# Performance work log

Measured on AMD Instinct MI355X. Metric: run time of the kernel, lower is better.

## Reference

```python
import jax, jax.numpy as jnp
import numpy as np

N_DRUG, N_MICROBE = 1500, 1572
N = N_DRUG + N_MICROBE          # 3072 nodes
F_IN = 1546                     # raw feature dim (fc1: 1546 -> 256)
D0 = 256                        # GCN input dim after fc1
H1 = H2 = 128                   # GCN hidden dims (H1 + H2 = 256)
B = 16384                       # number of (left,right) query pairs


def _sym_norm(A):
    # D^{-1/2} A D^{-1/2} (no self loops), zeros kept for isolated nodes
    deg = A.sum(axis=1)
    d = jnp.where(deg > 0, jax.lax.rsqrt(deg), 0.0)
    return A * d[:, None] * d[None, :]


def _compute_inf(adj, L):
    # dl.compute_inf: L-hop influence = L-th power of sym-normalized adjacency
    An = _sym_norm(adj)
    M = An
    for _ in range(L - 1):
        M = M @ An
    return M


def _gcn_norm(W):
    # GCNConv normalization: add self loops (weight 1), sym-normalize by weighted degree
    Ahat = W + jnp.eye(W.shape[0], dtype=W.dtype)
    deg = Ahat.sum(axis=1)
    d = jnp.where(deg > 0, jax.lax.rsqrt(deg), 0.0)
    return Ahat * d[:, None] * d[None, :]


def _glorot(key, shape):
    return jax.random.normal(key, shape, dtype=jnp.float32) / np.sqrt(shape[0])


def setup_inputs() -> dict:
    key = jax.random.key(0)
    ks = jax.random.split(key, 24)
    u = jax.random.uniform(ks[0], (N, N), dtype=jnp.float32)
    w = jax.random.uniform(ks[1], (N, N), dtype=jnp.float32)
    adj = jnp.where(u < 0.01, w, 0.0)
    adj = jnp.maximum(adj, adj.T)
    X = jax.random.normal(ks[2], (N, F_IN), dtype=jnp.float32)
    left = jax.random.randint(ks[3], (B,), 0, N)
    right = jax.random.randint(ks[4], (B,), 0, N)
    return dict(
        left=left, right=right, X=X, adj=adj, threshold=jnp.float32(1e-4),
        W_fc1=_glorot(ks[5], (F_IN, D0)), b_fc1=jnp.zeros((D0,), jnp.float32),
        Wg1=_glorot(ks[6], (D0, H1)), bg1=jnp.zeros((H1,), jnp.float32),
        Wg2=_glorot(ks[7], (H1, H2)), bg2=jnp.zeros((H2,), jnp.float32),
        Wg3=_glorot(ks[8], (D0, H1)), bg3=jnp.zeros((H1,), jnp.float32),
        Wg4=_glorot(ks[9], (H1, H2)), bg4=jnp.zeros((H2,), jnp.float32),
        Wg5=_glorot(ks[10], (D0, H1)), bg5=jnp.zeros((H1,), jnp.float32),
        Wg6=_glorot(ks[11], (H1, H2)), bg6=jnp.zeros((H2,), jnp.float32),
        cnn_k=jax.random.normal(ks[12], (1, 3, 3, 3), dtype=jnp.float32) * 0.1,
        cnn_b=jnp.zeros((1,), jnp.float32),
        W_a=_glorot(ks[13], (2 * (H1 + H2), 64)), b_a=jnp.zeros((64,), jnp.float32),
        W_b=_glorot(ks[14], (64, 2)), b_b=jnp.zeros((2,), jnp.float32),
    )


def reference(left, right, X, adj, threshold,
              W_fc1, b_fc1, Wg1, bg1, Wg2, bg2, Wg3, bg3, Wg4, bg4,
              Wg5, bg5, Wg6, bg6, cnn_k, cnn_b, W_a, b_a, W_b, b_b):
    X0 = jax.nn.relu(X @ W_fc1 + b_fc1)  # fc1: [N, 1546] -> [N, 256]

    def branch(mask_src, Wa, ba, Wb, bb):
        # dynamically thresholded edges carry the ORIGINAL adj weights
        Wadj = jnp.where(mask_src > threshold, adj, 0.0)
        An = _gcn_norm(Wadj)                       # [N, N]
        e1 = jax.nn.relu(An @ (X0 @ Wa) + ba)      # GCNConv 1
        e2 = jax.nn.relu(An @ (e1 @ Wb) + bb)      # GCNConv 2
        return jnp.concatenate([e1, e2], axis=1)   # [N, 256]

    emb_l2 = branch(_compute_inf(adj, 2), Wg1, bg1, Wg2, bg2)
    emb_l1 = branch(_compute_inf(adj, 1), Wg3, bg3, Wg4, bg4)
    emb_l0 = branch(adj, Wg5, bg5, Wg6, bg6)

    emb = jnp.stack([emb_l0, emb_l1, emb_l2], axis=0)[None]  # [1, 3, N, 256]
    conv = jax.lax.conv_general_dilated(
        emb, cnn_k, window_strides=(1, 1), padding=[(2, 2), (2, 2)],
        rhs_dilation=(2, 2), dimension_numbers=('NCHW', 'OIHW', 'NCHW'))
    emb_all = conv[0, 0] + cnn_b[0]                # [N, 256]

    pair = jnp.concatenate([emb_all[left], emb_all[right]], axis=1)  # [B, 512]
    h = jax.nn.relu(pair @ W_a + b_a)              # dropout is identity at eval
    logits = h @ W_b + b_b                         # [B, 2]
    return logits, emb_all
```

## Files before the change

kernel.cpp:

```cpp
#include <hip/hip_runtime.h>

#define NN 3072
#define FIN 1546
#define KP 1568
#define MAXR 192
#define KSPLIT 7
#define KSLICE 224

#define WSPLIT_BLOCKS (256 * KP / 256)
#define WGA_BLOCKS 384
#define CSR_BLOCKS (NN / 4)
#define FC1_BLOCKS (48 * 4 * KSPLIT)
#define RED_BLOCKS 768

typedef __attribute__((ext_vector_type(8))) __bf16 bf16x8;
typedef __attribute__((ext_vector_type(4))) __bf16 bf16x4;
typedef __attribute__((ext_vector_type(4))) float f32x4;

__global__ __launch_bounds__(256) void prep_k(const float* __restrict__ adj,
                                              int* __restrict__ cols, float* __restrict__ vals,
                                              int* __restrict__ cnt, float* __restrict__ dvec,
                                              const float* __restrict__ W,
                                              __bf16* __restrict__ WhT, __bf16* __restrict__ WlT,
                                              const float* __restrict__ Wga0,
                                              const float* __restrict__ Wga1,
                                              const float* __restrict__ Wga2,
                                              __bf16* __restrict__ WgaTh, __bf16* __restrict__ WgaTl) {
    int bid = blockIdx.x;
    if (bid < WSPLIT_BLOCKS) {
        int idx = bid * 256 + threadIdx.x;
        int c = idx / KP, k = idx - c * KP;
        float x = (k < FIN) ? W[(size_t)k * 256 + c] : 0.f;
        __bf16 h = (__bf16)x;
        WhT[idx] = h;
        WlT[idx] = (__bf16)(x - (float)h);
        return;
    }
    bid -= WSPLIT_BLOCKS;
    if (bid < WGA_BLOCKS) {
        int idx = bid * 256 + threadIdx.x;
        int b = idx >> 15, r = idx & 32767;
        int c = r >> 8, k = r & 255;
        const float* Wp = (b == 0) ? Wga0 : (b == 1) ? Wga1 : Wga2;
        float x = Wp[k * 128 + c];
        __bf16 h = (__bf16)x;
        WgaTh[idx] = h;
        WgaTl[idx] = (__bf16)(x - (float)h);
        return;
    }
    bid -= WGA_BLOCKS;
    int i = bid * 4 + (threadIdx.x >> 6);
    int lane = threadIdx.x & 63;
    const float* row = adj + (size_t)i * NN;
    unsigned long long below = (1ull << lane) - 1ull;
    float s = 0.f; int count = 0;
    int base = i * MAXR;
    float4 a4 = *(const float4*)(row + lane * 4);
    for (int c0 = 0; c0 < NN; c0 += 256) {
        float4 nxt;
        if (c0 + 256 < NN) nxt = *(const float4*)(row + c0 + 256 + lane * 4);
        float a[4] = {a4.x, a4.y, a4.z, a4.w};
        s += a[0] + a[1] + a[2] + a[3];
        unsigned long long bal[4];
        #pragma unroll
        for (int u = 0; u < 4; u++) bal[u] = __ballot(a[u] != 0.f);
        int before = 0;
        #pragma unroll
        for (int u = 0; u < 4; u++) before += __popcll(bal[u] & below);
        int local = 0;
        #pragma unroll
        for (int u = 0; u < 4; u++) {
            if (a[u] != 0.f) {
                int pos = count + before + local;
                if (pos < MAXR) { cols[base + pos] = c0 + lane * 4 + u; vals[base + pos] = a[u]; }
                local++;
            }
        }
        int tot = 0;
        #pragma unroll
        for (int u = 0; u < 4; u++) tot += __popcll(bal[u]);
        count += tot;
        a4 = nxt;
    }
    for (int off = 32; off; off >>= 1) s += __shfl_xor(s, off);
    if (lane == 0) {
        cnt[i] = count < MAXR ? count : MAXR;
        dvec[i] = (s > 0.f) ? 1.0f / sqrtf(s) : 0.f;
    }
}

__global__ __launch_bounds__(256) void fc1mask01_k(const float* __restrict__ X,
                                                   const __bf16* __restrict__ WhT,
                                                   const __bf16* __restrict__ WlT,
                                                   float* __restrict__ Cpart,
                                                   const int* __restrict__ cols,
                                                   const float* __restrict__ vals,
                                                   const int* __restrict__ cnt,
                                                   const float* __restrict__ dvec,
                                                   const float* __restrict__ thrp,
                                                   int* __restrict__ mcols,
                                                   float* __restrict__ mvals,
                                                   int* __restrict__ mcnt,
                                                   float* __restrict__ db) {
    __shared__ float ds[256];
    __shared__ int lcnt;
    int bid = blockIdx.x, tid = threadIdx.x;

    if (bid < FC1_BLOCKS) {
        int bx = bid % 48;
        int byz = bid / 48;
        int by = byz % 4, z = byz / 4;
        int w = tid >> 6, lane = tid & 63;
        int m = lane & 15, q = lane >> 4;
        int i0 = bx * 64, c0 = by * 64;
        int k0 = z * KSLICE;
        int rowA = i0 + w * 16 + m;
        const float* xrow = X + (size_t)rowA * FIN + k0 + q * 8;
        const __bf16* bh0 = WhT + (size_t)(c0 + m) * KP + k0 + q * 8;
        const __bf16* bl0 = WlT + (size_t)(c0 + m) * KP + k0 + q * 8;

        f32x4 acc[4];
        #pragma unroll
        for (int ct = 0; ct < 4; ct++)
            #pragma unroll
            for (int r = 0; r < 4; r++) acc[ct][r] = 0.f;

        #pragma unroll 2
        for (int ks = 0; ks < KSLICE; ks += 32) {
            float xv[8];
            if (z < KSPLIT - 1) {
                const float2* xp = (const float2*)(xrow + ks);
                float2 p0 = xp[0], p1 = xp[1], p2 = xp[2], p3 = xp[3];
                xv[0] = p0.x; xv[1] = p0.y; xv[2] = p1.x; xv[3] = p1.y;
                xv[4] = p2.x; xv[5] = p2.y; xv[6] = p3.x; xv[7] = p3.y;
            } else {
                int kb = k0 + q * 8 + ks;
                #pragma unroll
                for (int e = 0; e < 8; e++)
                    xv[e] = (kb + e < FIN) ? xrow[ks + e] : 0.f;
            }
            bf16x8 ah, al;
            #pragma unroll
            for (int e = 0; e < 8; e++) {
                __bf16 h = (__bf16)xv[e];
                ah[e] = h;
                al[e] = (__bf16)(xv[e] - (float)h);
            }
            #pragma unroll
            for (int ct = 0; ct < 4; ct++) {
                bf16x8 bh = *(const bf16x8*)(bh0 + (size_t)ct * 16 * KP + ks);
                bf16x8 bl = *(const bf16x8*)(bl0 + (size_t)ct * 16 * KP + ks);
                acc[ct] = __builtin_amdgcn_mfma_f32_16x16x32_bf16(ah, bh, acc[ct], 0, 0, 0);
                acc[ct] = __builtin_amdgcn_mfma_f32_16x16x32_bf16(ah, bl, acc[ct], 0, 0, 0);
                acc[ct] = __builtin_amdgcn_mfma_f32_16x16x32_bf16(al, bh, acc[ct], 0, 0, 0);
            }
        }
        float* outp = Cpart + (size_t)z * NN * 256;
        int rowBase = i0 + w * 16 + q * 4;
        #pragma unroll
        for (int ct = 0; ct < 4; ct++) {
            int col = c0 + ct * 16 + m;
            #pragma unroll
            for (int r = 0; r < 4; r++)
                outp[(size_t)(rowBase + r) * 256 + col] = acc[ct][r];
        }
        return;
    }

    int t = bid - FC1_BLOCKS;
    int mode = (t < NN) ? 0 : 1;
    int i = (t < NN) ? t : t - NN;

    mcols += (size_t)mode * NN * MAXR;
    mvals += (size_t)mode * NN * MAXR;
    mcnt  += (size_t)mode * NN;
    db    += (size_t)mode * NN;
    int ni = cnt[i], base = i * MAXR;
    float thr = *thrp;
    float di = dvec[i];

    if (tid == 0) lcnt = 0;
    __syncthreads();
    float s = 0.f;
    if (tid < ni) {
        int j = cols[base + tid];
        float a = vals[base + tid];
        float mv = (mode == 0) ? a : a * di * dvec[j];
        if (mv > thr) {
            int p = atomicAdd(&lcnt, 1);
            mcols[base + p] = j;
            mvals[base + p] = a;
            s = a;
        }
    }
    ds[tid] = s; __syncthreads();
    for (int off = 128; off; off >>= 1) {
        if (tid < off) ds[tid] += ds[tid + off];
        __syncthreads();
    }
    if (tid == 0) {
        mcnt[i] = lcnt;
        db[i] = 1.0f / sqrtf(ds[0] + 1.0f);
    }
}

__global__ __launch_bounds__(256) void redm2_k(const float* __restrict__ Cpart,
                                               const float* __restrict__ bias,
                                               __bf16* __restrict__ X0h,
                                               __bf16* __restrict__ X0l,
                                               const int* __restrict__ cols,
                                               const float* __restrict__ vals,
                                               const int* __restrict__ cnt,
                                               const float* __restrict__ dvec,
                                               const float* __restrict__ thrp,
                                               int* __restrict__ mcols,
                                               float* __restrict__ mvals,
                                               int* __restrict__ mcnt,
                                               float* __restrict__ db) {
    __shared__ float ds[NN];
    __shared__ int lcols[MAXR];
    __shared__ float lvals[MAXR];
    __shared__ int lcnt;
    __shared__ float osum;
    int bid = blockIdx.x, tid = threadIdx.x;

    if (bid < RED_BLOCKS) {
        int idx4 = bid * 256 + tid;
        int i = idx4 >> 6, c4 = (idx4 & 63) << 2;
        float4 s = ((const float4*)Cpart)[idx4];
        #pragma unroll
        for (int z = 1; z < KSPLIT; z++) {
            float4 t4 = ((const float4*)(Cpart + (size_t)z * NN * 256))[idx4];
            s.x += t4.x; s.y += t4.y; s.z += t4.z; s.w += t4.w;
        }
        float4 b = *(const float4*)&bias[c4];
        s.x = fmaxf(s.x + b.x, 0.f); s.y = fmaxf(s.y + b.y, 0.f);
        s.z = fmaxf(s.z + b.z, 0.f); s.w = fmaxf(s.w + b.w, 0.f);
        __bf16 h0 = (__bf16)s.x, h1 = (__bf16)s.y, h2 = (__bf16)s.z, h3 = (__bf16)s.w;
        bf16x4 hv = {h0, h1, h2, h3};
        bf16x4 lv = {(__bf16)(s.x - (float)h0), (__bf16)(s.y - (float)h1),
                     (__bf16)(s.z - (float)h2), (__bf16)(s.w - (float)h3)};
        *(bf16x4*)(X0h + (size_t)i * 256 + c4) = hv;
        *(bf16x4*)(X0l + (size_t)i * 256 + c4) = lv;
        return;
    }

    int i = bid - RED_BLOCKS;
    mcols += (size_t)2 * NN * MAXR;
    mvals += (size_t)2 * NN * MAXR;
    mcnt  += (size_t)2 * NN;
    db    += (size_t)2 * NN;
    int ni = cnt[i], base = i * MAXR;
    float thr = *thrp;
    float di = dvec[i];

    if (tid == 0) { osum = 0.f; lcnt = 0; }
    for (int j = tid; j < NN; j += 256) ds[j] = 0.f;
    __syncthreads();
    for (int t2 = tid; t2 < ni; t2 += 256) {
        int j = cols[base + t2];
        float a = vals[base + t2];
        lcols[t2] = j; lvals[t2] = a;
        ds[j] = a * dvec[j] * dvec[j];
    }
    __syncthreads();
    int lane = tid & 63, wv = tid >> 6;
    int sub = lane & 7, dg = lane >> 3;
    for (int o = wv * 8 + dg; o < ni; o += 32) {
        int j = lcols[o];
        int nj = cnt[j], bj = j * MAXR;
        float dot = 0.f;
        for (int t2 = sub; t2 < nj; t2 += 8)
            dot += vals[bj + t2] * ds[cols[bj + t2]];
        #pragma unroll
        for (int off = 4; off; off >>= 1) dot += __shfl_xor(dot, off);
        if (sub == 0 && di * dvec[j] * dot > thr) {
            int p = atomicAdd(&lcnt, 1);
            mcols[base + p] = j;
            mvals[base + p] = lvals[o];
            atomicAdd(&osum, lvals[o]);
        }
    }
    __syncthreads();
    if (tid == 0) {
        mcnt[i] = lcnt;
        db[i] = 1.0f / sqrtf(osum + 1.0f);
    }
}

__global__ __launch_bounds__(256) void gemm1_k(const __bf16* __restrict__ X0h,
                                               const __bf16* __restrict__ X0l,
                                               const __bf16* __restrict__ WgaTh,
                                               const __bf16* __restrict__ WgaTl,
                                               float* __restrict__ XWall) {
    int tid = threadIdx.x;
    int w = tid >> 6, lane = tid & 63;
    int m = lane & 15, q = lane >> 4;
    int i0 = blockIdx.x * 64, c0 = blockIdx.y * 64;
    int bz = blockIdx.z;
    int rowA = i0 + w * 16 + m;
    const __bf16* ah = X0h + (size_t)rowA * 256 + q * 8;
    const __bf16* al = X0l + (size_t)rowA * 256 + q * 8;
    const __bf16* bh0 = WgaTh + (size_t)bz * 128 * 256 + (size_t)(c0 + m) * 256 + q * 8;
    const __bf16* bl0 = WgaTl + (size_t)bz * 128 * 256 + (size_t)(c0 + m) * 256 + q * 8;

    f32x4 acc[4];
    #pragma unroll
    for (int ct = 0; ct < 4; ct++)
        #pragma unroll
        for (int r = 0; r < 4; r++) acc[ct][r] = 0.f;

    for (int ks = 0; ks < 256; ks += 32) {
        bf16x8 a_h = *(const bf16x8*)(ah + ks);
        bf16x8 a_l = *(const bf16x8*)(al + ks);
        #pragma unroll
        for (int ct = 0; ct < 4; ct++) {
            bf16x8 b_h = *(const bf16x8*)(bh0 + (size_t)ct * 16 * 256 + ks);
            bf16x8 b_l = *(const bf16x8*)(bl0 + (size_t)ct * 16 * 256 + ks);
            acc[ct] = __builtin_amdgcn_mfma_f32_16x16x32_bf16(a_h, b_h, acc[ct], 0, 0, 0);
            acc[ct] = __builtin_amdgcn_mfma_f32_16x16x32_bf16(a_h, b_l, acc[ct], 0, 0, 0);
            acc[ct] = __builtin_amdgcn_mfma_f32_16x16x32_bf16(a_l, b_h, acc[ct], 0, 0, 0);
        }
    }
    float* outp = XWall + (size_t)bz * NN * 128;
    int rowBase = i0 + w * 16 + q * 4;
    #pragma unroll
    for (int ct = 0; ct < 4; ct++) {
        int col = c0 + ct * 16 + m;
        #pragma unroll
        for (int r = 0; r < 4; r++)
            outp[(size_t)(rowBase + r) * 128 + col] = acc[ct][r];
    }
}

__global__ __launch_bounds__(256) void spmm3_k(const int* __restrict__ mcols,
                                               const float* __restrict__ mvals,
                                               const int* __restrict__ mcnt,
                                               const float* __restrict__ db,
                                               const float* __restrict__ Xin,
                                               const float* __restrict__ bias0,
                                               const float* __restrict__ bias1,
                                               const float* __restrict__ bias2,
                                               float* __restrict__ embf, int coff,
                                               const float* __restrict__ Wgb0,
                                               const float* __restrict__ Wgb1,
                                               const float* __restrict__ Wgb2,
                                               float* __restrict__ HW2out) {
    __shared__ float lcoef[MAXR];
    __shared__ int lj[MAXR];
    __shared__ float4 part[8][32];
    __shared__ float e1row[128];
    __shared__ float part2[2][128];
    int i = blockIdx.x, tid = threadIdx.x, b = blockIdx.y;
    mcols += (size_t)b * NN * MAXR;
    mvals += (size_t)b * NN * MAXR;
    mcnt  += (size_t)b * NN;
    db    += (size_t)b * NN;
    const float* Xb = Xin + (size_t)b * NN * 128;
    const float* bias = (b == 0) ? bias0 : (b == 1) ? bias1 : bias2;
    float dbi = db[i];
    int n = mcnt[i], base = i * MAXR;
    if (tid < n) {
        int j = mcols[base + tid];
        lj[tid] = j;
        lcoef[tid] = mvals[base + tid] * dbi * db[j];
    }
    __syncthreads();
    int g = tid >> 5, c4 = (tid & 31) << 2;
    float4 acc = make_float4(0.f, 0.f, 0.f, 0.f);
    float4 acc2 = make_float4(0.f, 0.f, 0.f, 0.f);
    if (g == 0) {
        float4 x = *(const float4*)&Xb[(size_t)i * 128 + c4];
        float d2 = dbi * dbi;
        acc = make_float4(d2 * x.x, d2 * x.y, d2 * x.z, d2 * x.w);
    }
    int t = g;
    for (; t + 8 < n; t += 16) {
        float cf0 = lcoef[t];
        float4 x0 = *(const float4*)&Xb[(size_t)lj[t] * 128 + c4];
        float cf1 = lcoef[t + 8];
        float4 x1 = *(const float4*)&Xb[(size_t)lj[t + 8] * 128 + c4];
        acc.x += cf0 * x0.x; acc.y += cf0 * x0.y; acc.z += cf0 * x0.z; acc.w += cf0 * x0.w;
        acc2.x += cf1 * x1.x; acc2.y += cf1 * x1.y; acc2.z += cf1 * x1.z; acc2.w += cf1 * x1.w;
    }
    if (t < n) {
        float cf = lcoef[t];
        float4 x = *(const float4*)&Xb[(size_t)lj[t] * 128 + c4];
        acc.x += cf * x.x; acc.y += cf * x.y; acc.z += cf * x.z; acc.w += cf * x.w;
    }
    acc.x += acc2.x; acc.y += acc2.y; acc.z += acc2.z; acc.w += acc2.w;
    part[g][tid & 31] = acc;
    __syncthreads();
    if (tid < 32) {
        float4 s = part[0][tid];
        #pragma unroll
        for (int gg = 1; gg < 8; gg++) {
            float4 t4 = part[gg][tid];
            s.x += t4.x; s.y += t4.y; s.z += t4.z; s.w += t4.w;
        }
        int cc = tid << 2;
        float4 bv = *(const float4*)&bias[cc];
        s.x = fmaxf(s.x + bv.x, 0.f); s.y = fmaxf(s.y + bv.y, 0.f);
        s.z = fmaxf(s.z + bv.z, 0.f); s.w = fmaxf(s.w + bv.w, 0.f);
        *(float4*)&embf[((size_t)b * NN + i) * 256 + coff + cc] = s;
        *(float4*)&e1row[cc] = s;
    }
    if (!HW2out) return;
    __syncthreads();
    int o = tid & 127, h = tid >> 7;
    const float* Wg = (b == 0) ? Wgb0 : (b == 1) ? Wgb1 : Wgb2;
    float ha = 0.f;
    int kbase = h * 64;
    const float* wp = Wg + (size_t)kbase * 128 + o;
    #pragma unroll 8
    for (int kk = 0; kk < 64; kk++)
        ha += e1row[kbase + kk] * wp[(size_t)kk * 128];
    part2[h][o] = ha;
    __syncthreads();
    if (tid < 128)
        HW2out[((size_t)b * NN + i) * 128 + tid] = part2[0][tid] + part2[1][tid];
}

__global__ __launch_bounds__(256) void convuv_k(const float* __restrict__ emb,
                                                const float* __restrict__ ck,
                                                const float* __restrict__ cb,
                                                float* __restrict__ outf,
                                                const float* __restrict__ Wa,
                                                float* __restrict__ uvp) {
    __shared__ float rows[3][3][256];
    __shared__ float embrow[256];
    __shared__ float part2[2][128];
    int n = blockIdx.x, c = threadIdx.x;
    #pragma unroll
    for (int i = 0; i < 3; i++)
        #pragma unroll
        for (int kh = 0; kh < 3; kh++) {
            int nn2 = n + 2 * kh - 2;
            rows[i][kh][c] = (nn2 >= 0 && nn2 < NN) ? emb[((size_t)i * NN + nn2) * 256 + c] : 0.f;
        }
    __syncthreads();
    float s = cb[0];
    #pragma unroll
    for (int i = 0; i < 3; i++)
        #pragma unroll
        for (int kh = 0; kh < 3; kh++)
            #pragma unroll
            for (int kw = 0; kw < 3; kw++) {
                int cc = c + 2 * kw - 2;
                if (cc >= 0 && cc < 256)
                    s += rows[i][kh][cc] * ck[(i * 3 + kh) * 3 + kw];
            }
    size_t idx = (size_t)n * 256 + c;
    outf[idx] = s;
    embrow[c] = s;
    __syncthreads();
    int o = c & 127, h = c >> 7;
    int kbase = h * 128;
    const float* wp = (o < 64) ? (Wa + (size_t)kbase * 64 + o)
                               : (Wa + (size_t)(256 + kbase) * 64 + (o - 64));
    float acc = 0.f;
    #pragma unroll 8
    for (int kk = 0; kk < 128; kk++)
        acc += embrow[kbase + kk] * wp[(size_t)kk * 64];
    part2[h][o] = acc;
    __syncthreads();
    if (c < 128)
        uvp[(size_t)n * 128 + c] = part2[0][c] + part2[1][c];
}

__global__ __launch_bounds__(256) void pairuv_k(const int* __restrict__ left,
                                                const int* __restrict__ right,
                                                const float* __restrict__ uvp,
                                                const float* __restrict__ ba,
                                                const float* __restrict__ Wb,
                                                const float* __restrict__ bb,
                                                float* __restrict__ out) {
    int tid = threadIdx.x;
    int w = tid >> 6, c = tid & 63;
    int base = blockIdx.x * 16 + w * 4;
    float bac = ba[c];
    float w0 = Wb[c * 2], w1 = Wb[c * 2 + 1];
    float b0 = bb[0], b1 = bb[1];
    #pragma unroll
    for (int pp = 0; pp < 4; pp++) {
        int row = base + pp;
        int l = left[row], r = right[row];
        float h = uvp[(size_t)l * 128 + c] + uvp[(size_t)r * 128 + 64 + c] + bac;
        h = fmaxf(h, 0.f);
        float s0 = h * w0, s1 = h * w1;
        for (int off = 32; off; off >>= 1) {
            s0 += __shfl_xor(s0, off);
            s1 += __shfl_xor(s1, off);
        }
        if (c == 0) {
            out[row * 2]     = s0 + b0;
            out[row * 2 + 1] = s1 + b1;
        }
    }
}

extern "C" void kernel_launch(void* const* d_in, const int* in_sizes, int n_in,
                              void* d_out, int out_size, void* d_ws, size_t ws_size,
                              hipStream_t stream) {
    const int* left  = (const int*)d_in[0];
    const int* right = (const int*)d_in[1];
    const float* X    = (const float*)d_in[2];
    const float* adj  = (const float*)d_in[3];
    const float* thr  = (const float*)d_in[4];
    const float* Wfc1 = (const float*)d_in[5];
    const float* bfc1 = (const float*)d_in[6];
    const float* Wga[3] = { (const float*)d_in[15], (const float*)d_in[11], (const float*)d_in[7] };
    const float* bga[3] = { (const float*)d_in[16], (const float*)d_in[12], (const float*)d_in[8] };
    const float* Wgb[3] = { (const float*)d_in[17], (const float*)d_in[13], (const float*)d_in[9] };
    const float* bgb[3] = { (const float*)d_in[18], (const float*)d_in[14], (const float*)d_in[10] };
    const float* cnnk = (const float*)d_in[19];
    const float* cnnb = (const float*)d_in[20];
    const float* Wa_  = (const float*)d_in[21];
    const float* ba_  = (const float*)d_in[22];
    const float* Wb_  = (const float*)d_in[23];
    const float* bb_  = (const float*)d_in[24];

    char* p = (char*)d_ws;
    auto take = [&](size_t n) { char* q = p; p += (n + 255) & ~(size_t)255; return q; };
    float* dvec = (float*)take(NN * 4);
    float* db3  = (float*)take((size_t)3 * NN * 4);
    int*   cnt  = (int*)take(NN * 4);
    int*   mcnt3 = (int*)take((size_t)3 * NN * 4);
    int*   cols = (int*)take((size_t)NN * MAXR * 4);
    float* vals = (float*)take((size_t)NN * MAXR * 4);
    int*   mcols3 = (int*)take((size_t)3 * NN * MAXR * 4);
    float* mvals3 = (float*)take((size_t)3 * NN * MAXR * 4);
    float* Cpart = (float*)take((size_t)KSPLIT * NN * 256 * 4);
    __bf16* X0h  = (__bf16*)take((size_t)NN * 256 * 2);
    __bf16* X0l  = (__bf16*)take((size_t)NN * 256 * 2);
    float* XWall = (float*)take((size_t)3 * NN * 128 * 4);
    float* HW2all= (float*)take((size_t)3 * NN * 128 * 4);
    float* embf  = (float*)take((size_t)3 * NN * 256 * 4);
    __bf16* WhT  = (__bf16*)take((size_t)256 * KP * 2);
    __bf16* WlT  = (__bf16*)take((size_t)256 * KP * 2);
    __bf16* WgaTh = (__bf16*)take((size_t)3 * 128 * 256 * 2);
    __bf16* WgaTl = (__bf16*)take((size_t)3 * 128 * 256 * 2);
    float* uvp   = (float*)take((size_t)NN * 128 * 4);

    float* out_logits = (float*)d_out;
    float* out_emb = out_logits + 32768;

    prep_k<<<WSPLIT_BLOCKS + WGA_BLOCKS + CSR_BLOCKS, 256, 0, stream>>>(
        adj, cols, vals, cnt, dvec, Wfc1, WhT, WlT,
        Wga[0], Wga[1], Wga[2], WgaTh, WgaTl);

    fc1mask01_k<<<FC1_BLOCKS + 2 * NN, 256, 0, stream>>>(
        X, WhT, WlT, Cpart,
        cols, vals, cnt, dvec, thr, mcols3, mvals3, mcnt3, db3);

    redm2_k<<<RED_BLOCKS + NN, 256, 0, stream>>>(
        Cpart, bfc1, X0h, X0l,
        cols, vals, cnt, dvec, thr, mcols3, mvals3, mcnt3, db3);

    gemm1_k<<<dim3(NN / 64, 2, 3), 256, 0, stream>>>(X0h, X0l, WgaTh, WgaTl, XWall);

    spmm3_k<<<dim3(NN, 3), 256, 0, stream>>>(mcols3, mvals3, mcnt3, db3, XWall,
                                             bga[0], bga[1], bga[2], embf, 0,
                                             Wgb[0], Wgb[1], Wgb[2], HW2all);

    spmm3_k<<<dim3(NN, 3), 256, 0, stream>>>(mcols3, mvals3, mcnt3, db3, HW2all,
                                             bgb[0], bgb[1], bgb[2], embf, 128,
                                             (const float*)0, (const float*)0, (const float*)0,
                                             (float*)0);

    convuv_k<<<NN, 256, 0, stream>>>(embf, cnnk, cnnb, out_emb, Wa_, uvp);

    pairuv_k<<<16384 / 16, 256, 0, stream>>>(left, right, uvp, ba_, Wb_, bb_, out_logits);
}
```

Baseline: 305.4 us.

## Move 2-hop mask construction into fc1 kernel and vectorize neighbor dot

The 2-hop influence mask computation moves out of the reduction kernel and into the fc1 split-K kernel launch, so it overlaps with the fc1 GEMM blocks. The reduction kernel shrinks to a pure split-K reduce plus bf16 split. The inner sparse dot now reads cols and vals in int4/float4 chunks. In exchange, the fc1 kernel's shared memory grows to about 14KB per block, which may lower occupancy for the GEMM blocks.

```diff
diff --git a/kernel.cpp b/kernel.cpp
--- a/kernel.cpp
+++ b/kernel.cpp
@@ -89,21 +89,24 @@
     }
 }
 
-__global__ __launch_bounds__(256) void fc1mask01_k(const float* __restrict__ X,
-                                                   const __bf16* __restrict__ WhT,
-                                                   const __bf16* __restrict__ WlT,
-                                                   float* __restrict__ Cpart,
-                                                   const int* __restrict__ cols,
-                                                   const float* __restrict__ vals,
-                                                   const int* __restrict__ cnt,
-                                                   const float* __restrict__ dvec,
-                                                   const float* __restrict__ thrp,
-                                                   int* __restrict__ mcols,
-                                                   float* __restrict__ mvals,
-                                                   int* __restrict__ mcnt,
-                                                   float* __restrict__ db) {
-    __shared__ float ds[256];
+__global__ __launch_bounds__(256) void fc1maskall_k(const float* __restrict__ X,
+                                                    const __bf16* __restrict__ WhT,
+                                                    const __bf16* __restrict__ WlT,
+                                                    float* __restrict__ Cpart,
+                                                    const int* __restrict__ cols,
+                                                    const float* __restrict__ vals,
+                                                    const int* __restrict__ cnt,
+                                                    const float* __restrict__ dvec,
+                                                    const float* __restrict__ thrp,
+                                                    int* __restrict__ mcols,
+                                                    float* __restrict__ mvals,
+                                                    int* __restrict__ mcnt,
+                                                    float* __restrict__ db) {
+    __shared__ float ds[NN];
+    __shared__ int lcols[MAXR];
+    __shared__ float lvals[MAXR];
     __shared__ int lcnt;
+    __shared__ float osum;
     int bid = blockIdx.x, tid = threadIdx.x;
 
     if (bid < FC1_BLOCKS) {
@@ -168,6 +171,61 @@
     }
 
     int t = bid - FC1_BLOCKS;
+    float thr = *thrp;
+
+    if (t < NN) {
+        int i = t;
+        mcols += (size_t)2 * NN * MAXR;
+        mvals += (size_t)2 * NN * MAXR;
+        mcnt  += (size_t)2 * NN;
+        db    += (size_t)2 * NN;
+        int ni = cnt[i], base = i * MAXR;
+        float di = dvec[i];
+
+        if (tid == 0) { osum = 0.f; lcnt = 0; }
+        for (int j = tid; j < NN; j += 256) ds[j] = 0.f;
+        __syncthreads();
+        for (int t2 = tid; t2 < ni; t2 += 256) {
+            int j = cols[base + t2];
+            float a = vals[base + t2];
+            lcols[t2] = j; lvals[t2] = a;
+            ds[j] = a * dvec[j] * dvec[j];
+        }
+        __syncthreads();
+        int lane = tid & 63, wv = tid >> 6;
+        int sub = lane & 7, dg = lane >> 3;
+        for (int o = wv * 8 + dg; o < ni; o += 32) {
+            int j = lcols[o];
+            int nj = cnt[j], bj = j * MAXR;
+            float dot = 0.f;
+            int nv = nj & ~3;
+            for (int t2 = sub * 4; t2 < nv; t2 += 32) {
+                int4 c4 = *(const int4*)&cols[bj + t2];
+                float4 v4 = *(const float4*)&vals[bj + t2];
+                dot += v4.x * ds[c4.x] + v4.y * ds[c4.y]
+                     + v4.z * ds[c4.z] + v4.w * ds[c4.w];
+            }
+            if (sub == 0)
+                for (int t2 = nv; t2 < nj; t2++)
+                    dot += vals[bj + t2] * ds[cols[bj + t2]];
+            #pragma unroll
+            for (int off = 4; off; off >>= 1) dot += __shfl_xor(dot, off);
+            if (sub == 0 && di * dvec[j] * dot > thr) {
+                int p = atomicAdd(&lcnt, 1);
+                mcols[base + p] = j;
+                mvals[base + p] = lvals[o];
+                atomicAdd(&osum, lvals[o]);
+            }
+        }
+        __syncthreads();
+        if (tid == 0) {
+            mcnt[i] = lcnt;
+            db[i] = 1.0f / sqrtf(osum + 1.0f);
+        }
+        return;
+    }
+
+    t -= NN;
     int mode = (t < NN) ? 0 : 1;
     int i = (t < NN) ? t : t - NN;
 
@@ -176,7 +234,6 @@
     mcnt  += (size_t)mode * NN;
     db    += (size_t)mode * NN;
     int ni = cnt[i], base = i * MAXR;
-    float thr = *thrp;
     float di = dvec[i];
 
     if (tid == 0) lcnt = 0;
@@ -204,88 +261,27 @@
     }
 }
 
-__global__ __launch_bounds__(256) void redm2_k(const float* __restrict__ Cpart,
-                                               const float* __restrict__ bias,
-                                               __bf16* __restrict__ X0h,
-                                               __bf16* __restrict__ X0l,
-                                               const int* __restrict__ cols,
-                                               const float* __restrict__ vals,
-                                               const int* __restrict__ cnt,
-                                               const float* __restrict__ dvec,
-                                               const float* __restrict__ thrp,
-                                               int* __restrict__ mcols,
-                                               float* __restrict__ mvals,
-                                               int* __restrict__ mcnt,
-                                               float* __restrict__ db) {
-    __shared__ float ds[NN];
-    __shared__ int lcols[MAXR];
-    __shared__ float lvals[MAXR];
-    __shared__ int lcnt;
-    __shared__ float osum;
-    int bid = blockIdx.x, tid = threadIdx.x;
-
-    if (bid < RED_BLOCKS) {
-        int idx4 = bid * 256 + tid;
-        int i = idx4 >> 6, c4 = (idx4 & 63) << 2;
-        float4 s = ((const float4*)Cpart)[idx4];
-        #pragma unroll
-        for (int z = 1; z < KSPLIT; z++) {
-            float4 t4 = ((const float4*)(Cpart + (size_t)z * NN * 256))[idx4];
-            s.x += t4.x; s.y += t4.y; s.z += t4.z; s.w += t4.w;
-        }
-        float4 b = *(const float4*)&bias[c4];
-        s.x = fmaxf(s.x + b.x, 0.f); s.y = fmaxf(s.y + b.y, 0.f);
-        s.z = fmaxf(s.z + b.z, 0.f); s.w = fmaxf(s.w + b.w, 0.f);
-        __bf16 h0 = (__bf16)s.x, h1 = (__bf16)s.y, h2 = (__bf16)s.z, h3 = (__bf16)s.w;
-        bf16x4 hv = {h0, h1, h2, h3};
-        bf16x4 lv = {(__bf16)(s.x - (float)h0), (__bf16)(s.y - (float)h1),
-                     (__bf16)(s.z - (float)h2), (__bf16)(s.w - (float)h3)};
-        *(bf16x4*)(X0h + (size_t)i * 256 + c4) = hv;
-        *(bf16x4*)(X0l + (size_t)i * 256 + c4) = lv;
-        return;
-    }
-
-    int i = bid - RED_BLOCKS;
-    mcols += (size_t)2 * NN * MAXR;
-    mvals += (size_t)2 * NN * MAXR;
-    mcnt  += (size_t)2 * NN;
-    db    += (size_t)2 * NN;
-    int ni = cnt[i], base = i * MAXR;
-    float thr = *thrp;
-    float di = dvec[i];
-
-    if (tid == 0) { osum = 0.f; lcnt = 0; }
-    for (int j = tid; j < NN; j += 256) ds[j] = 0.f;
-    __syncthreads();
-    for (int t2 = tid; t2 < ni; t2 += 256) {
-        int j = cols[base + t2];
-        float a = vals[base + t2];
-        lcols[t2] = j; lvals[t2] = a;
-        ds[j] = a * dvec[j] * dvec[j];
-    }
-    __syncthreads();
-    int lane = tid & 63, wv = tid >> 6;
-    int sub = lane & 7, dg = lane >> 3;
-    for (int o = wv * 8 + dg; o < ni; o += 32) {
-        int j = lcols[o];
-        int nj = cnt[j], bj = j * MAXR;
-        float dot = 0.f;
-        for (int t2 = sub; t2 < nj; t2 += 8)
-            dot += vals[bj + t2] * ds[cols[bj + t2]];
-        #pragma unroll
-        for (int off = 4; off; off >>= 1) dot += __shfl_xor(dot, off);
-        if (sub == 0 && di * dvec[j] * dot > thr) {
-            int p = atomicAdd(&lcnt, 1);
-            mcols[base + p] = j;
-            mvals[base + p] = lvals[o];
-            atomicAdd(&osum, lvals[o]);
-        }
-    }
-    __syncthreads();
-    if (tid == 0) {
-        mcnt[i] = lcnt;
-        db[i] = 1.0f / sqrtf(osum + 1.0f);
-    }
+__global__ __launch_bounds__(256) void red_k(const float* __restrict__ Cpart,
+                                             const float* __restrict__ bias,
+                                             __bf16* __restrict__ X0h,
+                                             __bf16* __restrict__ X0l) {
+    int idx4 = blockIdx.x * 256 + threadIdx.x;
+    int i = idx4 >> 6, c4 = (idx4 & 63) << 2;
+    float4 s = ((const float4*)Cpart)[idx4];
+    #pragma unroll
+    for (int z = 1; z < KSPLIT; z++) {
+        float4 t4 = ((const float4*)(Cpart + (size_t)z * NN * 256))[idx4];
+        s.x += t4.x; s.y += t4.y; s.z += t4.z; s.w += t4.w;
+    }
+    float4 b = *(const float4*)&bias[c4];
+    s.x = fmaxf(s.x + b.x, 0.f); s.y = fmaxf(s.y + b.y, 0.f);
+    s.z = fmaxf(s.z + b.z, 0.f); s.w = fmaxf(s.w + b.w, 0.f);
+    __bf16 h0 = (__bf16)s.x, h1 = (__bf16)s.y, h2 = (__bf16)s.z, h3 = (__bf16)s.w;
+    bf16x4 hv = {h0, h1, h2, h3};
+    bf16x4 lv = {(__bf16)(s.x - (float)h0), (__bf16)(s.y - (float)h1),
+                 (__bf16)(s.z - (float)h2), (__bf16)(s.w - (float)h3)};
+    *(bf16x4*)(X0h + (size_t)i * 256 + c4) = hv;
+    *(bf16x4*)(X0l + (size_t)i * 256 + c4) = lv;
 }
 
 __global__ __launch_bounds__(256) void gemm1_k(const __bf16* __restrict__ X0h,
@@ -549,13 +545,11 @@
         adj, cols, vals, cnt, dvec, Wfc1, WhT, WlT,
         Wga[0], Wga[1], Wga[2], WgaTh, WgaTl);
 
-    fc1mask01_k<<<FC1_BLOCKS + 2 * NN, 256, 0, stream>>>(
+    fc1maskall_k<<<FC1_BLOCKS + 3 * NN, 256, 0, stream>>>(
         X, WhT, WlT, Cpart,
         cols, vals, cnt, dvec, thr, mcols3, mvals3, mcnt3, db3);
 
-    redm2_k<<<RED_BLOCKS + NN, 256, 0, stream>>>(
-        Cpart, bfc1, X0h, X0l,
-        cols, vals, cnt, dvec, thr, mcols3, mvals3, mcnt3, db3);
+    red_k<<<RED_BLOCKS, 256, 0, stream>>>(Cpart, bfc1, X0h, X0l);
 
     gemm1_k<<<dim3(NN / 64, 2, 3), 256, 0, stream>>>(X0h, X0l, WgaTh, WgaTl, XWall);
 
```

New measurement: 302.8 us. About the same (-0.8%).
